# Kernel optimization log

Measured on AMD Instinct MI355X. Metric: run time of the kernel, lower is better.

## Reference

```python
import jax, jax.numpy as jnp
import numpy as np
from itertools import product

D = 64          # dense grid extent per axis
B = 2           # batch size
N_PER = 65536
NF_IN = 3
NF = 32
EPS = 1e-5


def _ravel(c):
    # c: [Q,4] (b,x,y,z) -> unique linear key
    return ((c[:, 0] * D + c[:, 1]) * D + c[:, 2]) * D + c[:, 3]


def _build_indices():
    """Build active coords and rule-book index tables (numpy, host-side)."""
    rng = np.random.default_rng(0)
    parts = []
    for b in range(B):
        lin = rng.choice(D ** 3, size=N_PER, replace=False)
        x = lin // (D * D)
        y = (lin // D) % D
        z = lin % D
        parts.append(np.stack([np.full(N_PER, b), x, y, z], 1))
    coords = np.concatenate(parts, 0).astype(np.int64)  # [N,4]
    keys = _ravel(coords)
    order = np.argsort(keys)
    skeys = keys[order]

    def lookup(qc):
        valid = ((qc[:, 1:] >= 0) & (qc[:, 1:] < D)).all(1)
        qc2 = np.where(valid[:, None], qc, 0)
        qk = _ravel(qc2)
        pos = np.clip(np.searchsorted(skeys, qk), 0, len(skeys) - 1)
        found = valid & (skeys[pos] == qk)
        return np.where(found, order[pos], -1)

    # 3x3x3 submanifold rule-book: neighbor index per active site per offset
    offs3 = list(product((-1, 0, 1), repeat=3))
    nbr = np.stack([lookup(coords + np.array([0, dx, dy, dz]))
                    for dx, dy, dz in offs3], 1)  # [N,27]
    # 2x2x2 stride-2 conv: output sites = unique parent cells
    parents = np.unique(np.concatenate([coords[:, :1], coords[:, 1:] // 2], 1), axis=0)
    base = parents * np.array([1, 2, 2, 2])
    offs2 = list(product((0, 1), repeat=3))
    child = np.stack([lookup(base + np.array([0, dx, dy, dz]))
                      for dx, dy, dz in offs2], 1)  # [M,8]
    return nbr.astype(np.int32), child.astype(np.int32)


def setup_inputs() -> dict:
    nbr, child = _build_indices()
    N = nbr.shape[0]
    key = jax.random.key(0)
    ks = jax.random.split(key, 6)

    def w(k, shape, fan):
        return jax.random.normal(k, shape, jnp.float32) / np.float32(np.sqrt(fan))

    ones = jnp.ones((NF,), jnp.float32)
    zeros = jnp.zeros((NF,), jnp.float32)
    return {
        "feats": jax.random.normal(ks[0], (N, NF_IN), jnp.float32),
        "nbr_idx": jnp.asarray(nbr),
        "child_idx": jnp.asarray(child),
        "W1": w(ks[1], (27, NF_IN, NF), 27 * NF_IN),
        "W2a": w(ks[2], (27, NF, NF), 27 * NF),
        "W2b": w(ks[3], (27, NF, NF), 27 * NF),
        "W3": w(ks[4], (8, NF, NF), 8 * NF),
        "g1": ones, "b1": zeros,
        "g2": ones, "b2": zeros,
        "g3": ones, "b3": zeros,
        "g4": ones, "b4": zeros,
    }


def _gconv(feats, idx, W):
    # sparse conv as rule-book gather -> per-offset GEMM -> accumulate
    mask = (idx >= 0)
    g = feats[jnp.clip(idx, 0)] * mask[..., None].astype(feats.dtype)  # [N,K,C]
    return jnp.einsum('nkc,kcd->nd', g, W)


def _bnrelu(x, g, b):
    # training-mode BN over active sites, then ReLU (scn.BatchNormReLU)
    mu = x.mean(0)
    var = x.var(0)
    return jax.nn.relu((x - mu) * jax.lax.rsqrt(var + EPS) * g + b)


def reference(feats, nbr_idx, child_idx, W1, W2a, W2b, W3,
              g1, b1, g2, b2, g3, b3, g4, b4):
    x1 = _gconv(feats, nbr_idx, W1)                       # p1: submanifold 3^3
    br = _gconv(_bnrelu(x1, g1, b1), nbr_idx, W2a)        # p2 residual branch
    br = _gconv(_bnrelu(br, g2, b2), nbr_idx, W2b)
    ft2 = _bnrelu(x1 + br, g3, b3)                        # AddTable + BNReLU
    x3 = _gconv(ft2, child_idx, W3)                       # p3: 2^3 stride-2 conv
    out = _bnrelu(x3, g4, b4)
    return (out, ft2)
```

## Files before the change

### kernel.cpp

```cpp
#include <hip/hip_runtime.h>
#include <hip/hip_bf16.h>


typedef __bf16 bf16_8 __attribute__((ext_vector_type(8)));
typedef float  f32x4  __attribute__((ext_vector_type(4)));

#define EPSV 1e-5f
#define NCOPY 32
#define CBLK 256

__device__ inline bf16_8 bzero8() {
    bf16_8 z;
#pragma unroll
    for (int i = 0; i < 8; ++i) z[i] = (__bf16)0.f;
    return z;
}

__device__ inline bf16_8 gatherrow(const __bf16* __restrict__ src, int nb, int kh) {
    bf16_8 a = *(const bf16_8*)(src + (size_t)(nb < 0 ? 0 : nb) * 32 + kh * 8);
    if (nb < 0) a = bzero8();
    return a;
}

__global__ __launch_bounds__(256) void k_cnt(const int* __restrict__ child, int m8,
                                             int* __restrict__ blockCnt) {
    __shared__ int ws[4];
    const int b = blockIdx.x, tid = threadIdx.x;
    const int chunk = (m8 + CBLK - 1) / CBLK;
    const int s0 = b * chunk, s1 = min(s0 + chunk, m8);
    int c = 0;
    for (int s = s0 + tid; s < s1; s += 256) c += (child[s] >= 0);
#pragma unroll
    for (int d = 1; d < 64; d <<= 1) c += __shfl_xor(c, d);
    if ((tid & 63) == 0) ws[tid >> 6] = c;
    __syncthreads();
    if (tid == 0) blockCnt[b] = ws[0] + ws[1] + ws[2] + ws[3];
}

__global__ __launch_bounds__(256) void k_compact(const int* __restrict__ child, int m8,
                                                 const int* __restrict__ blockCnt,
                                                 int* __restrict__ perm,
                                                 int* __restrict__ invperm) {
    __shared__ int woff[4];
    __shared__ int sbase;
    const int b = blockIdx.x, tid = threadIdx.x;
    const int chunk = (m8 + CBLK - 1) / CBLK;
    const int s0 = b * chunk, s1 = min(s0 + chunk, m8);
    if (tid == 0) {
        int a = 0;
        for (int i = 0; i < b; ++i) a += blockCnt[i];
        sbase = a;
    }
    __syncthreads();
    int off = sbase;
    for (int base = s0; base < s1; base += 256) {
        const int s = base + tid;
        int c = -1;
        bool v = false;
        if (s < s1) { c = child[s]; v = (c >= 0); }
        unsigned long long m = __ballot(v);
        if ((tid & 63) == 0) woff[tid >> 6] = __popcll(m);
        __syncthreads();
        const int wv = tid >> 6;
        int wpre = 0;
#pragma unroll
        for (int i = 0; i < 4; ++i) if (i < wv) wpre += woff[i];
        const int tot = woff[0] + woff[1] + woff[2] + woff[3];
        const int rank = __popcll(m & ((1ULL << (tid & 63)) - 1ULL));
        if (v) {
            const int pos = off + wpre + rank;
            perm[pos] = c;
            invperm[c] = pos;
        }
        off += tot;
        __syncthreads();
    }
}

__global__ __launch_bounds__(256) void k_reindex(
    const int* __restrict__ nbr, const int* __restrict__ child,
    const int* __restrict__ perm, const int* __restrict__ invperm,
    const float* __restrict__ feats,
    const float* __restrict__ W1, const float* __restrict__ W2a,
    const float* __restrict__ W2b, const float* __restrict__ W3,
    int* __restrict__ nbrP, int* __restrict__ childP, __bf16* __restrict__ fb,
    __bf16* __restrict__ w1t, __bf16* __restrict__ w2at,
    __bf16* __restrict__ w2bt, __bf16* __restrict__ w3t,
    float* __restrict__ statsAll, int n27, int m8, int n32) {
    int t = blockIdx.x * 256 + threadIdx.x;
    if (t < n27) {
        const int p = t / 27, k = t - p * 27;
        const int v = nbr[(size_t)perm[p] * 27 + k];
        nbrP[t] = (v < 0) ? -1 : invperm[v];
        return;
    }
    t -= n27;
    if (t < m8) {
        const int v = child[t];
        childP[t] = (v < 0) ? -1 : invperm[v];
        return;
    }
    t -= m8;
    if (t < n32) {
        const int p = t >> 5, c = t & 31;
        fb[t] = (c < 3) ? (__bf16)feats[(size_t)perm[p] * 3 + c] : (__bf16)0.f;
        return;
    }
    t -= n32;
    if (t < 27648) {
        const int k = t >> 10, r = t & 1023, d = r >> 5, c = r & 31;
        w1t[t] = (c < 3) ? (__bf16)W1[(k * 3 + c) * 32 + d] : (__bf16)0.f;
    } else if (t < 2 * 27648) {
        const int j = t - 27648;
        const int k = j >> 10, r = j & 1023, d = r >> 5, c = r & 31;
        w2at[j] = (__bf16)W2a[(k * 32 + c) * 32 + d];
    } else if (t < 3 * 27648) {
        const int j = t - 2 * 27648;
        const int k = j >> 10, r = j & 1023, d = r >> 5, c = r & 31;
        w2bt[j] = (__bf16)W2b[(k * 32 + c) * 32 + d];
    } else if (t < 3 * 27648 + 8192) {
        const int j = t - 3 * 27648;
        const int k = j >> 10, r = j & 1023, d = r >> 5, c = r & 31;
        w3t[j] = (__bf16)W3[(k * 32 + c) * 32 + d];
    } else if (t < 3 * 27648 + 8192 + 4 * NCOPY * 64) {
        statsAll[t - 3 * 27648 - 8192] = 0.f;
    }
}

template <int KOFF, bool ADD>
__global__ __launch_bounds__(256, 4) void k_conv(
    const __bf16* __restrict__ src,
    const int* __restrict__ idx,
    const __bf16* __restrict__ Wt,
    const __bf16* __restrict__ addsrc,
    __bf16* __restrict__ dst,
    float* __restrict__ spart_out,
    int nout) {
    constexpr int KPW = (KOFF + 3) / 4;
    __shared__ float part[4][32][34];
    __shared__ float lst[64];

    const int tid = threadIdx.x;
    const int lane = tid & 63;
    const int wv = tid >> 6;
    const int base = blockIdx.x * 32;
    const int sl = lane & 15;
    const int kh = lane >> 4;
    const int kbeg = wv * KPW;

    if (tid < 64) lst[tid] = 0.f;

    int nb[2][KPW];
#pragma unroll
    for (int g = 0; g < 2; ++g) {
        const int s = base + g * 16 + sl;
        const bool v = (s < nout);
        const int* ip = idx + (size_t)(v ? s : 0) * KOFF;
#pragma unroll
        for (int j = 0; j < KPW; ++j) {
            const bool kv = (kbeg + j) < KOFF;
            int t = ip[kv ? (kbeg + j) : 0];
            nb[g][j] = (v && kv) ? t : -1;
        }
    }

    bf16_8 av[2][KPW];
#pragma unroll
    for (int j = 0; j < KPW; ++j)
#pragma unroll
        for (int g = 0; g < 2; ++g)
            av[g][j] = gatherrow(src, nb[g][j], kh);
    __builtin_amdgcn_sched_barrier(0);

    f32x4 acc[2][2];
#pragma unroll
    for (int g = 0; g < 2; ++g)
#pragma unroll
        for (int h = 0; h < 2; ++h)
#pragma unroll
            for (int r = 0; r < 4; ++r) acc[g][h][r] = 0.f;

#pragma unroll
    for (int j = 0; j < KPW; ++j) {
        int kk = kbeg + j;
        if (kk > KOFF - 1) kk = KOFF - 1;
        bf16_8 b0 = *(const bf16_8*)(Wt + kk * 1024 + sl * 32 + kh * 8);
        bf16_8 b1 = *(const bf16_8*)(Wt + kk * 1024 + (16 + sl) * 32 + kh * 8);
        acc[0][0] = __builtin_amdgcn_mfma_f32_16x16x32_bf16(av[0][j], b0, acc[0][0], 0, 0, 0);
        acc[0][1] = __builtin_amdgcn_mfma_f32_16x16x32_bf16(av[0][j], b1, acc[0][1], 0, 0, 0);
        acc[1][0] = __builtin_amdgcn_mfma_f32_16x16x32_bf16(av[1][j], b0, acc[1][0], 0, 0, 0);
        acc[1][1] = __builtin_amdgcn_mfma_f32_16x16x32_bf16(av[1][j], b1, acc[1][1], 0, 0, 0);
    }

#pragma unroll
    for (int g = 0; g < 2; ++g)
#pragma unroll
        for (int h = 0; h < 2; ++h)
#pragma unroll
            for (int r = 0; r < 4; ++r)
                part[wv][g * 16 + kh * 4 + r][h * 16 + sl] = acc[g][h][r];
    __syncthreads();

    if (tid < 128) {
        const int sloc = tid >> 2;
        const int c0 = (tid & 3) * 8;
        float v[8];
#pragma unroll
        for (int i = 0; i < 8; ++i)
            v[i] = part[0][sloc][c0 + i] + part[1][sloc][c0 + i] +
                   part[2][sloc][c0 + i] + part[3][sloc][c0 + i];
        const int site = base + sloc;
        if (site < nout) {
            if (ADD) {
                bf16_8 ad = *(const bf16_8*)(addsrc + (size_t)site * 32 + c0);
#pragma unroll
                for (int i = 0; i < 8; ++i) v[i] += (float)ad[i];
            }
            bf16_8 o;
#pragma unroll
            for (int i = 0; i < 8; ++i) o[i] = (__bf16)v[i];
            *(bf16_8*)(dst + (size_t)site * 32 + c0) = o;
        } else {
#pragma unroll
            for (int i = 0; i < 8; ++i) v[i] = 0.f;
        }
        float sv[8], qv[8];
#pragma unroll
        for (int i = 0; i < 8; ++i) { sv[i] = v[i]; qv[i] = v[i] * v[i]; }
#pragma unroll
        for (int d = 4; d < 64; d <<= 1) {
#pragma unroll
            for (int i = 0; i < 8; ++i) {
                sv[i] += __shfl_xor(sv[i], d);
                qv[i] += __shfl_xor(qv[i], d);
            }
        }
        if ((lane & 60) == 0) {
#pragma unroll
            for (int i = 0; i < 8; ++i) {
                atomicAdd(&lst[c0 + i], sv[i]);
                atomicAdd(&lst[32 + c0 + i], qv[i]);
            }
        }
    }
    __syncthreads();
    if (tid < 64)
        atomicAdd(&spart_out[(blockIdx.x & (NCOPY - 1)) * 64 + tid], lst[tid]);
}

template <bool WF32, bool WBF>
__global__ __launch_bounds__(256) void k_bn(
    const __bf16* __restrict__ src, const float* __restrict__ spart,
    const float* __restrict__ gamma, const float* __restrict__ beta,
    float inv_cnt, int nrows,
    __bf16* __restrict__ dstb, float* __restrict__ dstf,
    const int* __restrict__ permw) {
    __shared__ float ss[64];
    __shared__ float sc[32], sh[32];
    const int tid = threadIdx.x;
    if (tid < 64) {
        float a = 0.f;
#pragma unroll
        for (int i = 0; i < NCOPY; ++i) a += spart[i * 64 + tid];
        ss[tid] = a;
    }
    __syncthreads();
    if (tid < 32) {
        float mu = ss[tid] * inv_cnt;
        float var = ss[32 + tid] * inv_cnt - mu * mu;
        float s = gamma[tid] * rsqrtf(var + EPSV);
        sc[tid] = s;
        sh[tid] = beta[tid] - mu * s;
    }
    __syncthreads();
    const int gtid = blockIdx.x * blockDim.x + tid;
    const int c0 = (gtid & 3) * 8;
    float scale[8], shift[8];
#pragma unroll
    for (int i = 0; i < 8; ++i) { scale[i] = sc[c0 + i]; shift[i] = sh[c0 + i]; }
    const int rstride = (gridDim.x * blockDim.x) >> 2;
    for (int r = gtid >> 2; r < nrows; r += rstride) {
        const size_t off = (size_t)r * 32 + c0;
        bf16_8 v = *(const bf16_8*)(src + off);
        float y[8];
#pragma unroll
        for (int i = 0; i < 8; ++i) y[i] = fmaxf(fmaf((float)v[i], scale[i], shift[i]), 0.f);
        if (WBF) {
            bf16_8 o;
#pragma unroll
            for (int i = 0; i < 8; ++i) o[i] = (__bf16)y[i];
            *(bf16_8*)(dstb + off) = o;
        }
        if (WF32) {
            f32x4 lo, hi;
#pragma unroll
            for (int i = 0; i < 4; ++i) { lo[i] = y[i]; hi[i] = y[4 + i]; }
            const size_t woff = permw ? ((size_t)permw[r] * 32 + c0) : off;
            *(f32x4*)(dstf + woff) = lo;
            *(f32x4*)(dstf + woff + 4) = hi;
        }
    }
}

extern "C" void kernel_launch(void* const* d_in, const int* in_sizes, int n_in,
                              void* d_out, int out_size, void* d_ws, size_t ws_size,
                              hipStream_t stream) {
    const float* feats = (const float*)d_in[0];
    const int* nbr     = (const int*)d_in[1];
    const int* child   = (const int*)d_in[2];
    const float* W1  = (const float*)d_in[3];
    const float* W2a = (const float*)d_in[4];
    const float* W2b = (const float*)d_in[5];
    const float* W3  = (const float*)d_in[6];
    const float* g1 = (const float*)d_in[7];  const float* b1 = (const float*)d_in[8];
    const float* g2 = (const float*)d_in[9];  const float* b2 = (const float*)d_in[10];
    const float* g3 = (const float*)d_in[11]; const float* b3 = (const float*)d_in[12];
    const float* g4 = (const float*)d_in[13]; const float* b4 = (const float*)d_in[14];

    const int N = in_sizes[0] / 3;
    const int M8 = in_sizes[2];
    const int M = M8 / 8;

    float* outp = (float*)d_out;
    float* ft2p = outp + (size_t)M * 32;

    char* ws = (char*)d_ws;
    float* statsAll = (float*)ws;
    __bf16* w1t  = (__bf16*)(ws + 32768);
    __bf16* w2at = w1t + 27648;
    __bf16* w2bt = w2at + 27648;
    __bf16* w3t  = w2bt + 27648;
    __bf16* X  = (__bf16*)(ws + 215040);
    __bf16* T  = X + (size_t)N * 32;
    __bf16* FB = T + (size_t)N * 32;
    char* p2 = ws + 215040 + 3 * (size_t)N * 64;
    int* perm    = (int*)p2;
    int* invperm = perm + N;
    int* nbrP    = invperm + N;
    int* childP  = nbrP + (size_t)N * 27;
    int* blockCnt = childP + M8;

    float* s1 = statsAll;
    float* s2 = statsAll + NCOPY * 64;
    float* s3 = statsAll + 2 * NCOPY * 64;
    float* s4 = statsAll + 3 * NCOPY * 64;

    k_cnt<<<CBLK, 256, 0, stream>>>(child, M8, blockCnt);
    k_compact<<<CBLK, 256, 0, stream>>>(child, M8, blockCnt, perm, invperm);

    const int n27 = N * 27, n32 = N * 32;
    const int rtot = n27 + M8 + n32 + 3 * 27648 + 8192 + 4 * NCOPY * 64;
    k_reindex<<<(rtot + 255) / 256, 256, 0, stream>>>(
        nbr, child, perm, invperm, feats, W1, W2a, W2b, W3,
        nbrP, childP, FB, w1t, w2at, w2bt, w3t, statsAll, n27, M8, n32);

    const int cgrid = (N + 31) / 32;
    const int cgrid3 = (M + 31) / 32;
    const float invN = 1.f / N, invM = 1.f / M;

    k_conv<27, false><<<cgrid, 256, 0, stream>>>(FB, nbrP, w1t, nullptr, X, s1, N);
    k_bn<false, true><<<1024, 256, 0, stream>>>(X, s1, g1, b1, invN, N, T, nullptr, nullptr);
    k_conv<27, false><<<cgrid, 256, 0, stream>>>(T, nbrP, w2at, nullptr, FB, s2, N);
    k_bn<false, true><<<1024, 256, 0, stream>>>(FB, s2, g2, b2, invN, N, T, nullptr, nullptr);
    k_conv<27, true><<<cgrid, 256, 0, stream>>>(T, nbrP, w2bt, X, FB, s3, N);
    k_bn<true, true><<<1024, 256, 0, stream>>>(FB, s3, g3, b3, invN, N, T, ft2p, perm);
    k_conv<8, false><<<cgrid3, 256, 0, stream>>>(T, childP, w3t, nullptr, X, s4, M);
    k_bn<true, false><<<1024, 256, 0, stream>>>(X, s4, g4, b4, invM, M, nullptr, outp, nullptr);
}
```

Baseline: 193.8 us.

## Transpose rule-book indices to offset-major and use zero sentinel row

Neighbor and child index tables are rebuilt in offset-major layout, padded to a multiple of four offsets and to a multiple of 32 outputs, so that each conv wave reads indices with coalesced loads. Missing neighbors now point to an extra zeroed feature row at index N instead of -1, and the weights are padded with a zero offset slice. This removes the per-gather branch, the clamping and the bounds checks from the conv inner loops. The cost is slightly more workspace, and the grid of N/32 assumes N is divisible by 32.

New measurement: 181.2 us. 6.5% less time.

```diff
diff --git a/kernel.cpp b/kernel.cpp
--- a/kernel.cpp
+++ b/kernel.cpp
@@ -8,19 +8,6 @@
 #define EPSV 1e-5f
 #define NCOPY 32
 #define CBLK 256
-
-__device__ inline bf16_8 bzero8() {
-    bf16_8 z;
-#pragma unroll
-    for (int i = 0; i < 8; ++i) z[i] = (__bf16)0.f;
-    return z;
-}
-
-__device__ inline bf16_8 gatherrow(const __bf16* __restrict__ src, int nb, int kh) {
-    bf16_8 a = *(const bf16_8*)(src + (size_t)(nb < 0 ? 0 : nb) * 32 + kh * 8);
-    if (nb < 0) a = bzero8();
-    return a;
-}
 
 __global__ __launch_bounds__(256) void k_cnt(const int* __restrict__ child, int m8,
                                              int* __restrict__ blockCnt) {
@@ -83,60 +70,86 @@
     const float* __restrict__ feats,
     const float* __restrict__ W1, const float* __restrict__ W2a,
     const float* __restrict__ W2b, const float* __restrict__ W3,
-    int* __restrict__ nbrP, int* __restrict__ childP, __bf16* __restrict__ fb,
+    int* __restrict__ nbrT, int* __restrict__ childT,
+    __bf16* __restrict__ X, __bf16* __restrict__ T, __bf16* __restrict__ FB,
     __bf16* __restrict__ w1t, __bf16* __restrict__ w2at,
     __bf16* __restrict__ w2bt, __bf16* __restrict__ w3t,
-    float* __restrict__ statsAll, int n27, int m8, int n32) {
+    float* __restrict__ statsAll,
+    int N, int M, int MP) {
     int t = blockIdx.x * 256 + threadIdx.x;
-    if (t < n27) {
-        const int p = t / 27, k = t - p * 27;
-        const int v = nbr[(size_t)perm[p] * 27 + k];
-        nbrP[t] = (v < 0) ? -1 : invperm[v];
-        return;
-    }
-    t -= n27;
-    if (t < m8) {
-        const int v = child[t];
-        childP[t] = (v < 0) ? -1 : invperm[v];
-        return;
-    }
-    t -= m8;
-    if (t < n32) {
+    if (t < 28 * N) {
+        const int k = t / N, p = t - k * N;
+        int o = N;
+        if (k < 27) {
+            const int v = nbr[(size_t)perm[p] * 27 + k];
+            o = (v < 0) ? N : invperm[v];
+        }
+        nbrT[t] = o;
+        return;
+    }
+    t -= 28 * N;
+    if (t < 8 * MP) {
+        const int k = t / MP, m = t - k * MP;
+        int o = N;
+        if (m < M) {
+            const int v = child[(size_t)m * 8 + k];
+            o = (v < 0) ? N : invperm[v];
+        }
+        childT[t] = o;
+        return;
+    }
+    t -= 8 * MP;
+    if (t < N * 32) {
         const int p = t >> 5, c = t & 31;
-        fb[t] = (c < 3) ? (__bf16)feats[(size_t)perm[p] * 3 + c] : (__bf16)0.f;
-        return;
-    }
-    t -= n32;
-    if (t < 27648) {
+        FB[t] = (c < 3) ? (__bf16)feats[(size_t)perm[p] * 3 + c] : (__bf16)0.f;
+        return;
+    }
+    t -= N * 32;
+    if (t < 96) {
+        const int b = t >> 5, c = t & 31;
+        __bf16* p = (b == 0) ? X : (b == 1) ? T : FB;
+        p[(size_t)N * 32 + c] = (__bf16)0.f;
+        return;
+    }
+    t -= 96;
+    if (t < 28672) {
         const int k = t >> 10, r = t & 1023, d = r >> 5, c = r & 31;
-        w1t[t] = (c < 3) ? (__bf16)W1[(k * 3 + c) * 32 + d] : (__bf16)0.f;
-    } else if (t < 2 * 27648) {
-        const int j = t - 27648;
-        const int k = j >> 10, r = j & 1023, d = r >> 5, c = r & 31;
-        w2at[j] = (__bf16)W2a[(k * 32 + c) * 32 + d];
-    } else if (t < 3 * 27648) {
-        const int j = t - 2 * 27648;
-        const int k = j >> 10, r = j & 1023, d = r >> 5, c = r & 31;
-        w2bt[j] = (__bf16)W2b[(k * 32 + c) * 32 + d];
-    } else if (t < 3 * 27648 + 8192) {
-        const int j = t - 3 * 27648;
-        const int k = j >> 10, r = j & 1023, d = r >> 5, c = r & 31;
-        w3t[j] = (__bf16)W3[(k * 32 + c) * 32 + d];
-    } else if (t < 3 * 27648 + 8192 + 4 * NCOPY * 64) {
-        statsAll[t - 3 * 27648 - 8192] = 0.f;
-    }
+        w1t[t] = (k < 27 && c < 3) ? (__bf16)W1[(k * 3 + c) * 32 + d] : (__bf16)0.f;
+        return;
+    }
+    t -= 28672;
+    if (t < 28672) {
+        const int k = t >> 10, r = t & 1023, d = r >> 5, c = r & 31;
+        w2at[t] = (k < 27) ? (__bf16)W2a[(k * 32 + c) * 32 + d] : (__bf16)0.f;
+        return;
+    }
+    t -= 28672;
+    if (t < 28672) {
+        const int k = t >> 10, r = t & 1023, d = r >> 5, c = r & 31;
+        w2bt[t] = (k < 27) ? (__bf16)W2b[(k * 32 + c) * 32 + d] : (__bf16)0.f;
+        return;
+    }
+    t -= 28672;
+    if (t < 8192) {
+        const int k = t >> 10, r = t & 1023, d = r >> 5, c = r & 31;
+        w3t[t] = (__bf16)W3[(k * 32 + c) * 32 + d];
+        return;
+    }
+    t -= 8192;
+    if (t < 4 * NCOPY * 64) statsAll[t] = 0.f;
 }
 
 template <int KOFF, bool ADD>
 __global__ __launch_bounds__(256, 4) void k_conv(
     const __bf16* __restrict__ src,
-    const int* __restrict__ idx,
+    const int* __restrict__ idxT,
     const __bf16* __restrict__ Wt,
     const __bf16* __restrict__ addsrc,
     __bf16* __restrict__ dst,
     float* __restrict__ spart_out,
-    int nout) {
-    constexpr int KPW = (KOFF + 3) / 4;
+    int nout, int npad) {
+    constexpr int KPAD = ((KOFF + 3) / 4) * 4;
+    constexpr int KPW = KPAD / 4;
     __shared__ float part[4][32][34];
     __shared__ float lst[64];
 
@@ -152,24 +165,17 @@
 
     int nb[2][KPW];
 #pragma unroll
-    for (int g = 0; g < 2; ++g) {
-        const int s = base + g * 16 + sl;
-        const bool v = (s < nout);
-        const int* ip = idx + (size_t)(v ? s : 0) * KOFF;
-#pragma unroll
-        for (int j = 0; j < KPW; ++j) {
-            const bool kv = (kbeg + j) < KOFF;
-            int t = ip[kv ? (kbeg + j) : 0];
-            nb[g][j] = (v && kv) ? t : -1;
-        }
-    }
+    for (int j = 0; j < KPW; ++j)
+#pragma unroll
+        for (int g = 0; g < 2; ++g)
+            nb[g][j] = idxT[(kbeg + j) * npad + base + g * 16 + sl];
 
     bf16_8 av[2][KPW];
 #pragma unroll
     for (int j = 0; j < KPW; ++j)
 #pragma unroll
         for (int g = 0; g < 2; ++g)
-            av[g][j] = gatherrow(src, nb[g][j], kh);
+            av[g][j] = *(const bf16_8*)(src + (size_t)nb[g][j] * 32 + kh * 8);
     __builtin_amdgcn_sched_barrier(0);
 
     f32x4 acc[2][2];
@@ -182,8 +188,7 @@
 
 #pragma unroll
     for (int j = 0; j < KPW; ++j) {
-        int kk = kbeg + j;
-        if (kk > KOFF - 1) kk = KOFF - 1;
+        const int kk = kbeg + j;
         bf16_8 b0 = *(const bf16_8*)(Wt + kk * 1024 + sl * 32 + kh * 8);
         bf16_8 b1 = *(const bf16_8*)(Wt + kk * 1024 + (16 + sl) * 32 + kh * 8);
         acc[0][0] = __builtin_amdgcn_mfma_f32_16x16x32_bf16(av[0][j], b0, acc[0][0], 0, 0, 0);
@@ -320,6 +325,7 @@
     const int N = in_sizes[0] / 3;
     const int M8 = in_sizes[2];
     const int M = M8 / 8;
+    const int MP = ((M + 31) / 32) * 32;
 
     float* outp = (float*)d_out;
     float* ft2p = outp + (size_t)M * 32;
@@ -327,18 +333,18 @@
     char* ws = (char*)d_ws;
     float* statsAll = (float*)ws;
     __bf16* w1t  = (__bf16*)(ws + 32768);
-    __bf16* w2at = w1t + 27648;
-    __bf16* w2bt = w2at + 27648;
-    __bf16* w3t  = w2bt + 27648;
-    __bf16* X  = (__bf16*)(ws + 215040);
-    __bf16* T  = X + (size_t)N * 32;
-    __bf16* FB = T + (size_t)N * 32;
-    char* p2 = ws + 215040 + 3 * (size_t)N * 64;
+    __bf16* w2at = w1t + 28672;
+    __bf16* w2bt = w2at + 28672;
+    __bf16* w3t  = w2bt + 28672;
+    __bf16* X  = (__bf16*)(ws + 221184);
+    __bf16* T  = X + (size_t)(N + 1) * 32;
+    __bf16* FB = T + (size_t)(N + 1) * 32;
+    char* p2 = (char*)(FB + (size_t)(N + 1) * 32);
     int* perm    = (int*)p2;
     int* invperm = perm + N;
-    int* nbrP    = invperm + N;
-    int* childP  = nbrP + (size_t)N * 27;
-    int* blockCnt = childP + M8;
+    int* nbrT    = invperm + N;
+    int* childT  = nbrT + (size_t)28 * N;
+    int* blockCnt = childT + (size_t)8 * MP;
 
     float* s1 = statsAll;
     float* s2 = statsAll + NCOPY * 64;
@@ -348,22 +354,21 @@
     k_cnt<<<CBLK, 256, 0, stream>>>(child, M8, blockCnt);
     k_compact<<<CBLK, 256, 0, stream>>>(child, M8, blockCnt, perm, invperm);
 
-    const int n27 = N * 27, n32 = N * 32;
-    const int rtot = n27 + M8 + n32 + 3 * 27648 + 8192 + 4 * NCOPY * 64;
+    const int rtot = 28 * N + 8 * MP + N * 32 + 96 + 3 * 28672 + 8192 + 4 * NCOPY * 64;
     k_reindex<<<(rtot + 255) / 256, 256, 0, stream>>>(
         nbr, child, perm, invperm, feats, W1, W2a, W2b, W3,
-        nbrP, childP, FB, w1t, w2at, w2bt, w3t, statsAll, n27, M8, n32);
-
-    const int cgrid = (N + 31) / 32;
-    const int cgrid3 = (M + 31) / 32;
+        nbrT, childT, X, T, FB, w1t, w2at, w2bt, w3t, statsAll, N, M, MP);
+
+    const int cgrid = N / 32;
+    const int cgrid3 = MP / 32;
     const float invN = 1.f / N, invM = 1.f / M;
 
-    k_conv<27, false><<<cgrid, 256, 0, stream>>>(FB, nbrP, w1t, nullptr, X, s1, N);
+    k_conv<27, false><<<cgrid, 256, 0, stream>>>(FB, nbrT, w1t, nullptr, X, s1, N, N);
     k_bn<false, true><<<1024, 256, 0, stream>>>(X, s1, g1, b1, invN, N, T, nullptr, nullptr);
-    k_conv<27, false><<<cgrid, 256, 0, stream>>>(T, nbrP, w2at, nullptr, FB, s2, N);
+    k_conv<27, false><<<cgrid, 256, 0, stream>>>(T, nbrT, w2at, nullptr, FB, s2, N, N);
     k_bn<false, true><<<1024, 256, 0, stream>>>(FB, s2, g2, b2, invN, N, T, nullptr, nullptr);
-    k_conv<27, true><<<cgrid, 256, 0, stream>>>(T, nbrP, w2bt, X, FB, s3, N);
+    k_conv<27, true><<<cgrid, 256, 0, stream>>>(T, nbrT, w2bt, X, FB, s3, N, N);
     k_bn<true, true><<<1024, 256, 0, stream>>>(FB, s3, g3, b3, invN, N, T, ft2p, perm);
-    k_conv<8, false><<<cgrid3, 256, 0, stream>>>(T, childP, w3t, nullptr, X, s4, M);
+    k_conv<8, false><<<cgrid3, 256, 0, stream>>>(T, childT, w3t, nullptr, X, s4, M, MP);
     k_bn<true, false><<<1024, 256, 0, stream>>>(X, s4, g4, b4, invM, M, nullptr, outp, nullptr);
 }
```
